# Kernel optimization log

Hardware: AMD Instinct MI355X
Metric: run time of the kernel (lower is better)

Reference implementation:

```python
import jax, jax.numpy as jnp
import numpy as np

B, S, HID = 1, 2048, 2048
H, KVH, HD = 32, 8, 64
THETA = 10000.0


def _rotate_half(x):
    x1, x2 = jnp.split(x, 2, axis=-1)
    return jnp.concatenate([-x2, x1], axis=-1)


def _rope_cos_sin(seq_len, head_dim, theta, dtype):
    inv_freq = 1.0 / (theta ** (jnp.arange(0, head_dim, 2, dtype=jnp.float32) / head_dim))
    pos = jnp.arange(seq_len, dtype=jnp.float32)
    freqs = pos[:, None] * inv_freq[None, :]          # [S, HD/2]
    emb = jnp.concatenate([freqs, freqs], axis=-1)     # [S, HD]
    return jnp.cos(emb).astype(dtype), jnp.sin(emb).astype(dtype)


def setup_inputs() -> dict:
    key = jax.random.key(0)
    k0, k1, k2, k3, k4 = jax.random.split(key, 5)
    w = lambda k, shape: jax.random.normal(k, shape, dtype=jnp.float32) * 0.02
    return {
        "hidden_states": jax.random.normal(k0, (B, S, HID), dtype=jnp.float32),
        "Wq": w(k1, (H * HD, HID)),
        "Wk": w(k2, (KVH * HD, HID)),
        "Wv": w(k3, (KVH * HD, HID)),
        "Wo": w(k4, (HID, H * HD)),
    }


def reference(hidden_states, Wq, Wk, Wv, Wo):
    b, s, _ = hidden_states.shape
    dtype = hidden_states.dtype

    # QKV projections (nn.Linear, bias=False -> x @ W.T)
    q = (hidden_states @ Wq.T).reshape(b, s, H, HD).transpose(0, 2, 1, 3)    # [b,H,s,d]
    k = (hidden_states @ Wk.T).reshape(b, s, KVH, HD).transpose(0, 2, 1, 3)  # [b,KVH,s,d]
    v = (hidden_states @ Wv.T).reshape(b, s, KVH, HD).transpose(0, 2, 1, 3)

    # RoPE (prefill: position_ids = arange(s))
    cos, sin = _rope_cos_sin(s, HD, THETA, dtype)  # [s, HD]
    apply_rope = lambda x: x * cos + _rotate_half(x) * sin
    q = apply_rope(q)
    k = apply_rope(k)

    # GQA: repeat KV heads to match query heads
    groups = H // KVH
    k = jnp.repeat(k, groups, axis=1)  # [b,H,s,d]
    v = jnp.repeat(v, groups, axis=1)

    scale = 1.0 / jnp.sqrt(jnp.asarray(HD, dtype=dtype))
    logits = jnp.einsum('bhqd,bhkd->bhqk', q, k) * scale  # [b,H,s,s]

    # prefill causal mask (phys_past_len = 0)
    causal = jnp.tril(jnp.ones((s, s), dtype=bool))
    logits = jnp.where(causal, logits, jnp.finfo(dtype).min)

    attn = jax.nn.softmax(logits, axis=-1)
    out = jnp.einsum('bhqk,bhkd->bhqd', attn, v)            # [b,H,s,d]
    out = out.transpose(0, 2, 1, 3).reshape(b, s, H * HD)   # [b,s,hidden]
    return out @ Wo.T
```

## Files before the change

kernel.cpp:

```cpp
#include <hip/hip_runtime.h>
#include <hip/hip_bf16.h>
#include <cstdint>
#include <cstddef>

#define SEQ   2048
#define HID   2048
#define NH    32
#define NKVH  8
#define HD    64
#define KVDIM (NKVH * HD)

typedef __bf16 bf16_t;
typedef __bf16 bf16x8 __attribute__((ext_vector_type(8)));
typedef float  f32x4  __attribute__((ext_vector_type(4)));

#define ROPE_L 0.4152410118609203f

#if __has_builtin(__builtin_amdgcn_exp2f)
#define QSCALE 0.18033688011112043f
#define EXPFN(x) __builtin_amdgcn_exp2f(x)
#else
#define QSCALE 0.125f
#define EXPFN(x) __expf(x)
#endif

__device__ __forceinline__ bf16x8 load8(const float* p) {
    const float4 lo = *(const float4*)p;
    const float4 hi = *(const float4*)(p + 4);
    bf16x8 r;
    r[0] = (bf16_t)lo.x; r[1] = (bf16_t)lo.y; r[2] = (bf16_t)lo.z; r[3] = (bf16_t)lo.w;
    r[4] = (bf16_t)hi.x; r[5] = (bf16_t)hi.y; r[6] = (bf16_t)hi.z; r[7] = (bf16_t)hi.w;
    return r;
}

__device__ __forceinline__ void load_lds16(const bf16_t* g, bf16_t* l) {
    __builtin_amdgcn_global_load_lds((const __attribute__((address_space(1))) void*)g,
                                     (__attribute__((address_space(3))) void*)l,
                                     16, 0, 0);
}

#define NX  (SEQ * HID)
#define NWQ (NH * HD * HID)
#define NWK (KVDIM * HID)
#define NWV (KVDIM * HID)
#define NWO (HID * NH * HD)
#define NTOT (NX + NWQ + NWK + NWV + NWO)

__global__ __launch_bounds__(256) void cvt_all(const float* __restrict__ X,
                                               const float* __restrict__ Wq,
                                               const float* __restrict__ Wk,
                                               const float* __restrict__ Wv,
                                               const float* __restrict__ Wo,
                                               bf16_t* __restrict__ Xb,
                                               bf16_t* __restrict__ Wqb,
                                               bf16_t* __restrict__ Wkb,
                                               bf16_t* __restrict__ Wvb,
                                               bf16_t* __restrict__ Wob)
{
    size_t i = ((size_t)blockIdx.x * 256 + threadIdx.x) * 8;
    if (i >= NTOT) return;
    const size_t E0 = NX, E1 = E0 + NWQ, E2 = E1 + NWK, E3 = E2 + NWV;
    const float* s; bf16_t* d; size_t off;
    if (i < E0)      { s = X;  d = Xb;  off = i; }
    else if (i < E1) { s = Wq; d = Wqb; off = i - E0; }
    else if (i < E2) { s = Wk; d = Wkb; off = i - E1; }
    else if (i < E3) { s = Wv; d = Wvb; off = i - E2; }
    else             { s = Wo; d = Wob; off = i - E3; }
    *(bf16x8*)(d + off) = load8(s + off);
}

__global__ __launch_bounds__(256) void qkv_gemm(const bf16_t* __restrict__ Xb,
                                                const bf16_t* __restrict__ Wqb,
                                                const bf16_t* __restrict__ Wkb,
                                                const bf16_t* __restrict__ Wvb,
                                                bf16_t* __restrict__ Qb,
                                                bf16_t* __restrict__ Kb,
                                                bf16_t* __restrict__ Vt)
{
    __shared__ alignas(16) bf16_t sa[128 * 32];
    __shared__ alignas(16) bf16_t sb[64 * 32];
    const int t = threadIdx.x;
    const int lane = t & 63;
    const int w  = t >> 6;
    const int n16 = lane & 15;
    const int q4  = lane >> 4;
    f32x4 acc[2][4] = {};

    const int m0 = blockIdx.x * 128;
    const int n0 = blockIdx.y * 64;

    const bf16_t* B;
    int mode, nc;
    if (n0 < NH * HD)              { B = Wqb + (size_t)n0 * HID;                     mode = 0; nc = n0; }
    else if (n0 < NH * HD + KVDIM) { B = Wkb + (size_t)(n0 - NH * HD) * HID;         mode = 1; nc = n0 - NH * HD; }
    else                           { B = Wvb + (size_t)(n0 - NH * HD - KVDIM) * HID; mode = 2; nc = n0 - NH * HD - KVDIM; }

    const int lrow = lane >> 2;
    const int lcol = (lane & 3) * 8;
    const bf16_t* ag = Xb + (size_t)(m0 + w * 32 + lrow) * HID + lcol;
    const bf16_t* bg = B  + (size_t)(w * 16 + lrow) * HID + lcol;
    bf16_t* la0 = &sa[(w * 32) * 32];
    bf16_t* la1 = &sa[(w * 32 + 16) * 32];
    bf16_t* lb0 = &sb[(w * 16) * 32];

    for (int k0 = 0; k0 < HID; k0 += 32) {
        load_lds16(ag + k0, la0);
        load_lds16(ag + k0 + (size_t)16 * HID, la1);
        load_lds16(bg + k0, lb0);
        __syncthreads();
        bf16x8 bfrag[4];
#pragma unroll
        for (int j = 0; j < 4; ++j)
            bfrag[j] = *(const bf16x8*)&sb[(j * 16 + n16) * 32 + q4 * 8];
#pragma unroll
        for (int i = 0; i < 2; ++i) {
            bf16x8 af = *(const bf16x8*)&sa[(w * 32 + i * 16 + n16) * 32 + q4 * 8];
#pragma unroll
            for (int j = 0; j < 4; ++j)
                acc[i][j] = __builtin_amdgcn_mfma_f32_16x16x32_bf16(af, bfrag[j], acc[i][j], 0, 0, 0);
        }
        __syncthreads();
    }

    if (mode < 2) {
#pragma unroll
        for (int jt = 0; jt < 2; ++jt) {
            float dd = (float)(jt * 16 + n16);
            float inv = exp2f(-dd * ROPE_L);
#pragma unroll
            for (int i = 0; i < 2; ++i) {
#pragma unroll
                for (int r = 0; r < 4; ++r) {
                    int pos = m0 + w * 32 + i * 16 + q4 * 4 + r;
                    float ang = (float)pos * inv;
                    float sn, cs;
                    sincosf(ang, &sn, &cs);
                    float x1 = acc[i][jt][r], x2 = acc[i][jt + 2][r];
                    acc[i][jt][r]     = x1 * cs - x2 * sn;
                    acc[i][jt + 2][r] = x2 * cs + x1 * sn;
                }
            }
        }
        const float osc = (mode == 0) ? QSCALE : 1.0f;
        bf16_t* dst = (mode == 0) ? Qb : Kb;
        const int ld = (mode == 0) ? NH * HD : KVDIM;
#pragma unroll
        for (int i = 0; i < 2; ++i)
#pragma unroll
            for (int j = 0; j < 4; ++j) {
                int row = m0 + w * 32 + i * 16 + q4 * 4;
                int col = nc + j * 16 + n16;
#pragma unroll
                for (int r = 0; r < 4; ++r)
                    dst[(size_t)(row + r) * ld + col] = (bf16_t)(acc[i][j][r] * osc);
            }
    } else {
#pragma unroll
        for (int i = 0; i < 2; ++i)
#pragma unroll
            for (int j = 0; j < 4; ++j) {
                int row = m0 + w * 32 + i * 16 + q4 * 4;
                int col = nc + j * 16 + n16;
#pragma unroll
                for (int r = 0; r < 4; ++r)
                    Vt[(size_t)col * SEQ + row + r] = (bf16_t)acc[i][j][r];
            }
    }
}

__global__ __launch_bounds__(256) void o_gemm(const bf16_t* __restrict__ A,
                                              const bf16_t* __restrict__ Bw,
                                              float* __restrict__ C)
{
    __shared__ alignas(16) bf16_t sa[128 * 32];
    __shared__ alignas(16) bf16_t sb[64 * 32];
    const int t = threadIdx.x;
    const int lane = t & 63;
    const int w  = t >> 6;
    const int n16 = lane & 15;
    const int q4  = lane >> 4;
    f32x4 acc[2][4] = {};

    const int m0 = blockIdx.x * 128;
    const int n0 = blockIdx.y * 64;

    const int lrow = lane >> 2;
    const int lcol = (lane & 3) * 8;
    const bf16_t* ag = A  + (size_t)(m0 + w * 32 + lrow) * HID + lcol;
    const bf16_t* bg = Bw + (size_t)(n0 + w * 16 + lrow) * HID + lcol;
    bf16_t* la0 = &sa[(w * 32) * 32];
    bf16_t* la1 = &sa[(w * 32 + 16) * 32];
    bf16_t* lb0 = &sb[(w * 16) * 32];

    for (int k0 = 0; k0 < HID; k0 += 32) {
        load_lds16(ag + k0, la0);
        load_lds16(ag + k0 + (size_t)16 * HID, la1);
        load_lds16(bg + k0, lb0);
        __syncthreads();
        bf16x8 bfrag[4];
#pragma unroll
        for (int j = 0; j < 4; ++j)
            bfrag[j] = *(const bf16x8*)&sb[(j * 16 + n16) * 32 + q4 * 8];
#pragma unroll
        for (int i = 0; i < 2; ++i) {
            bf16x8 af = *(const bf16x8*)&sa[(w * 32 + i * 16 + n16) * 32 + q4 * 8];
#pragma unroll
            for (int j = 0; j < 4; ++j)
                acc[i][j] = __builtin_amdgcn_mfma_f32_16x16x32_bf16(af, bfrag[j], acc[i][j], 0, 0, 0);
        }
        __syncthreads();
    }

#pragma unroll
    for (int i = 0; i < 2; ++i)
#pragma unroll
        for (int j = 0; j < 4; ++j) {
            int row = m0 + w * 32 + i * 16 + q4 * 4;
            int col = n0 + j * 16 + n16;
#pragma unroll
            for (int r = 0; r < 4; ++r)
                C[(size_t)(row + r) * HID + col] = acc[i][j][r];
        }
}

__global__ __launch_bounds__(256) void attn_mfma(const bf16_t* __restrict__ Qm,
                                                 const bf16_t* __restrict__ Km,
                                                 const bf16_t* __restrict__ Vt,
                                                 bf16_t* __restrict__ Om)
{
    const int h   = blockIdx.x & (NH - 1);
    const int qt  = (SEQ / 64 - 1) - (blockIdx.x >> 5);
    const int q0  = qt * 64;
    const int kvh = h >> 2;
    const int t   = threadIdx.x;
    const int w   = t >> 6;
    const int lane = t & 63;
    const int n16 = lane & 15;
    const int q4  = lane >> 4;

    __shared__ alignas(16) bf16_t kA[128 * 32];
    __shared__ alignas(16) bf16_t kB[128 * 32];
    __shared__ alignas(16) bf16_t vc0[64 * 32], vc1[64 * 32];
    __shared__ alignas(16) bf16_t vc2[64 * 32], vc3[64 * 32];
    __shared__ alignas(16) bf16_t psA[4][16 * 32];
    __shared__ alignas(16) bf16_t psB[4][16 * 32];

    const int qrow = q0 + w * 16 + n16;
    const bf16_t* qbase = Qm + (size_t)qrow * HID + h * HD;
    const bf16x8 qf0 = *(const bf16x8*)(qbase + q4 * 8);
    const bf16x8 qf1 = *(const bf16x8*)(qbase + 32 + q4 * 8);

    f32x4 acc[4] = {};
    f32x4 acc_l = {};
    const bf16_t one = (bf16_t)1.0f;
    const bf16x8 ones8 = {one, one, one, one, one, one, one, one};

    const int srow = lane >> 2;
    const int scol = (lane & 3) * 8;
    const bf16_t* kg = Km + (size_t)kvh * HD + scol;
    const bf16_t* vg = Vt + (size_t)(kvh * HD) * SEQ;

    const int rowg0 = q0 + w * 16 + q4 * 4;
    const int nhalf = qt + 1;

    for (int kb = 0; kb * 2 < nhalf; ++kb) {
        const int k0 = kb * 128;
        {
            const int r0 = w * 16 + srow;
            const bf16_t* kp0 = kg + (size_t)(k0 + r0) * KVDIM;
            const bf16_t* kp1 = kg + (size_t)(k0 + 64 + r0) * KVDIM;
            load_lds16(kp0,      &kA[(w * 16) * 32]);
            load_lds16(kp0 + 32, &kB[(w * 16) * 32]);
            load_lds16(kp1,      &kA[(64 + w * 16) * 32]);
            load_lds16(kp1 + 32, &kB[(64 + w * 16) * 32]);
            const bf16_t* vp = vg + (size_t)r0 * SEQ + k0 + scol;
            load_lds16(vp,      &vc0[(w * 16) * 32]);
            load_lds16(vp + 32, &vc1[(w * 16) * 32]);
            load_lds16(vp + 64, &vc2[(w * 16) * 32]);
            load_lds16(vp + 96, &vc3[(w * 16) * 32]);
        }
        __syncthreads();

#pragma unroll
        for (int hh = 0; hh < 2; ++hh) {
            const int gh = 2 * kb + hh;
            if (gh >= nhalf) break;
            const bf16_t* kAh = &kA[hh * 64 * 32];
            const bf16_t* kBh = &kB[hh * 64 * 32];
            const bf16_t* vAh = hh ? vc2 : vc0;
            const bf16_t* vBh = hh ? vc3 : vc1;

            f32x4 st[4];
#pragma unroll
            for (int jt = 0; jt < 4; ++jt) {
                bf16x8 kf0 = *(const bf16x8*)&kAh[(jt * 16 + n16) * 32 + q4 * 8];
                bf16x8 kf1 = *(const bf16x8*)&kBh[(jt * 16 + n16) * 32 + q4 * 8];
                f32x4 s = {};
                s = __builtin_amdgcn_mfma_f32_16x16x32_bf16(qf0, kf0, s, 0, 0, 0);
                s = __builtin_amdgcn_mfma_f32_16x16x32_bf16(qf1, kf1, s, 0, 0, 0);
                st[jt] = s;
            }

            if (gh == qt) {
#pragma unroll
                for (int jt = 0; jt < 4; ++jt) {
                    int colg = gh * 64 + jt * 16 + n16;
#pragma unroll
                    for (int r = 0; r < 4; ++r)
                        if (colg > rowg0 + r) st[jt][r] = -1e30f;
                }
            }

#pragma unroll
            for (int jt = 0; jt < 4; ++jt)
#pragma unroll
                for (int r = 0; r < 4; ++r)
                    st[jt][r] = EXPFN(st[jt][r]);

#pragma unroll
            for (int jt = 0; jt < 4; ++jt) {
                bf16_t* ph = (jt < 2) ? psA[w] : psB[w];
                int c16 = (jt & 1) * 16;
#pragma unroll
                for (int r = 0; r < 4; ++r)
                    ph[(q4 * 4 + r) * 32 + c16 + n16] = (bf16_t)st[jt][r];
            }
            bf16x8 pf0 = *(const bf16x8*)&psA[w][n16 * 32 + q4 * 8];
            bf16x8 pf1 = *(const bf16x8*)&psB[w][n16 * 32 + q4 * 8];

            acc_l = __builtin_amdgcn_mfma_f32_16x16x32_bf16(pf0, ones8, acc_l, 0, 0, 0);
            acc_l = __builtin_amdgcn_mfma_f32_16x16x32_bf16(pf1, ones8, acc_l, 0, 0, 0);

#pragma unroll
            for (int jd = 0; jd < 4; ++jd) {
                bf16x8 vf0 = *(const bf16x8*)&vAh[(jd * 16 + n16) * 32 + q4 * 8];
                bf16x8 vf1 = *(const bf16x8*)&vBh[(jd * 16 + n16) * 32 + q4 * 8];
                acc[jd] = __builtin_amdgcn_mfma_f32_16x16x32_bf16(pf0, vf0, acc[jd], 0, 0, 0);
                acc[jd] = __builtin_amdgcn_mfma_f32_16x16x32_bf16(pf1, vf1, acc[jd], 0, 0, 0);
            }
        }
        __syncthreads();
    }

    float linv[4];
#pragma unroll
    for (int r = 0; r < 4; ++r) linv[r] = 1.0f / acc_l[r];
#pragma unroll
    for (int jd = 0; jd < 4; ++jd)
#pragma unroll
        for (int r = 0; r < 4; ++r) {
            int rowg = rowg0 + r;
            Om[(size_t)rowg * HID + h * HD + jd * 16 + n16] = (bf16_t)(acc[jd][r] * linv[r]);
        }
}

extern "C" void kernel_launch(void* const* d_in, const int* in_sizes, int n_in,
                              void* d_out, int out_size, void* d_ws, size_t ws_size,
                              hipStream_t stream)
{
    const float* X  = (const float*)d_in[0];
    const float* Wq = (const float*)d_in[1];
    const float* Wk = (const float*)d_in[2];
    const float* Wv = (const float*)d_in[3];
    const float* Wo = (const float*)d_in[4];
    float* out = (float*)d_out;

    bf16_t* Xb  = (bf16_t*)d_ws;
    bf16_t* Wqb = Xb  + (size_t)NX;
    bf16_t* Wkb = Wqb + (size_t)NWQ;
    bf16_t* Wvb = Wkb + (size_t)NWK;
    bf16_t* Wob = Wvb + (size_t)NWV;
    bf16_t* Qb  = Wob + (size_t)NWO;
    bf16_t* Kb  = Qb  + (size_t)SEQ * (NH * HD);
    bf16_t* Vt  = Kb  + (size_t)SEQ * KVDIM;
    bf16_t* Ob  = Vt  + (size_t)SEQ * KVDIM;

    dim3 blk(256);

    cvt_all<<<dim3((NTOT / 8 + 255) / 256), blk, 0, stream>>>(X, Wq, Wk, Wv, Wo, Xb, Wqb, Wkb, Wvb, Wob);

    qkv_gemm<<<dim3(SEQ / 128, (NH * HD + 2 * KVDIM) / 64), blk, 0, stream>>>(Xb, Wqb, Wkb, Wvb, Qb, Kb, Vt);

    attn_mfma<<<dim3((SEQ / 64) * NH), blk, 0, stream>>>(Qb, Kb, Vt, Ob);

    o_gemm<<<dim3(SEQ / 128, HID / 64), blk, 0, stream>>>(Ob, Wob, out);
}
```

Measured before the change: 214.7 us.

## Double K-step in GEMMs and use 128-row query tiles in attention

Both GEMMs now stage 64 columns of K per barrier pair, in two LDS sub-buffers, which halves the number of __syncthreads per tile. Attention now handles 128 query rows per block with 32 rows per wave, so each K/V tile loaded into LDS serves twice as many queries. It also interleaves long and short causal tiles in the block order to balance load, and swizzles the P staging buffer to cut LDS bank conflicts. The costs are more LDS and registers per block and fewer blocks overall, which launch_bounds(256,3) tries to keep at an acceptable occupancy.

```diff
diff --git a/kernel.cpp b/kernel.cpp
--- a/kernel.cpp
+++ b/kernel.cpp
@@ -77,8 +77,8 @@
                                                 bf16_t* __restrict__ Kb,
                                                 bf16_t* __restrict__ Vt)
 {
-    __shared__ alignas(16) bf16_t sa[128 * 32];
-    __shared__ alignas(16) bf16_t sb[64 * 32];
+    __shared__ alignas(16) bf16_t sa0[128 * 32], sa1[128 * 32];
+    __shared__ alignas(16) bf16_t sb0[64 * 32],  sb1[64 * 32];
     const int t = threadIdx.x;
     const int lane = t & 63;
     const int w  = t >> 6;
@@ -97,27 +97,38 @@
 
     const int lrow = lane >> 2;
     const int lcol = (lane & 3) * 8;
-    const bf16_t* ag = Xb + (size_t)(m0 + w * 32 + lrow) * HID + lcol;
+    const bf16_t* ag = Xb + (size_t)(m0 + w * 16 + lrow) * HID + lcol;
     const bf16_t* bg = B  + (size_t)(w * 16 + lrow) * HID + lcol;
-    bf16_t* la0 = &sa[(w * 32) * 32];
-    bf16_t* la1 = &sa[(w * 32 + 16) * 32];
-    bf16_t* lb0 = &sb[(w * 16) * 32];
-
-    for (int k0 = 0; k0 < HID; k0 += 32) {
-        load_lds16(ag + k0, la0);
-        load_lds16(ag + k0 + (size_t)16 * HID, la1);
-        load_lds16(bg + k0, lb0);
-        __syncthreads();
-        bf16x8 bfrag[4];
-#pragma unroll
-        for (int j = 0; j < 4; ++j)
-            bfrag[j] = *(const bf16x8*)&sb[(j * 16 + n16) * 32 + q4 * 8];
-#pragma unroll
-        for (int i = 0; i < 2; ++i) {
-            bf16x8 af = *(const bf16x8*)&sa[(w * 32 + i * 16 + n16) * 32 + q4 * 8];
+    bf16_t* la0  = &sa0[(w * 16) * 32];
+    bf16_t* la1  = &sa1[(w * 16) * 32];
+    bf16_t* la0b = &sa0[(64 + w * 16) * 32];
+    bf16_t* la1b = &sa1[(64 + w * 16) * 32];
+    bf16_t* lb0  = &sb0[(w * 16) * 32];
+    bf16_t* lb1  = &sb1[(w * 16) * 32];
+
+    for (int k0 = 0; k0 < HID; k0 += 64) {
+        load_lds16(ag + k0,                        la0);
+        load_lds16(ag + k0 + 32,                   la1);
+        load_lds16(ag + (size_t)64 * HID + k0,      la0b);
+        load_lds16(ag + (size_t)64 * HID + k0 + 32, la1b);
+        load_lds16(bg + k0,      lb0);
+        load_lds16(bg + k0 + 32, lb1);
+        __syncthreads();
+#pragma unroll
+        for (int kk = 0; kk < 2; ++kk) {
+            const bf16_t* sa = kk ? sa1 : sa0;
+            const bf16_t* sb = kk ? sb1 : sb0;
+            bf16x8 bfrag[4];
 #pragma unroll
             for (int j = 0; j < 4; ++j)
-                acc[i][j] = __builtin_amdgcn_mfma_f32_16x16x32_bf16(af, bfrag[j], acc[i][j], 0, 0, 0);
+                bfrag[j] = *(const bf16x8*)&sb[(j * 16 + n16) * 32 + q4 * 8];
+#pragma unroll
+            for (int i = 0; i < 2; ++i) {
+                bf16x8 af = *(const bf16x8*)&sa[(w * 32 + i * 16 + n16) * 32 + q4 * 8];
+#pragma unroll
+                for (int j = 0; j < 4; ++j)
+                    acc[i][j] = __builtin_amdgcn_mfma_f32_16x16x32_bf16(af, bfrag[j], acc[i][j], 0, 0, 0);
+            }
         }
         __syncthreads();
     }
@@ -172,8 +183,8 @@
                                               const bf16_t* __restrict__ Bw,
                                               float* __restrict__ C)
 {
-    __shared__ alignas(16) bf16_t sa[128 * 32];
-    __shared__ alignas(16) bf16_t sb[64 * 32];
+    __shared__ alignas(16) bf16_t sa0[128 * 32], sa1[128 * 32];
+    __shared__ alignas(16) bf16_t sb0[64 * 32],  sb1[64 * 32];
     const int t = threadIdx.x;
     const int lane = t & 63;
     const int w  = t >> 6;
@@ -186,27 +197,38 @@
 
     const int lrow = lane >> 2;
     const int lcol = (lane & 3) * 8;
-    const bf16_t* ag = A  + (size_t)(m0 + w * 32 + lrow) * HID + lcol;
+    const bf16_t* ag = A  + (size_t)(m0 + w * 16 + lrow) * HID + lcol;
     const bf16_t* bg = Bw + (size_t)(n0 + w * 16 + lrow) * HID + lcol;
-    bf16_t* la0 = &sa[(w * 32) * 32];
-    bf16_t* la1 = &sa[(w * 32 + 16) * 32];
-    bf16_t* lb0 = &sb[(w * 16) * 32];
-
-    for (int k0 = 0; k0 < HID; k0 += 32) {
-        load_lds16(ag + k0, la0);
-        load_lds16(ag + k0 + (size_t)16 * HID, la1);
-        load_lds16(bg + k0, lb0);
-        __syncthreads();
-        bf16x8 bfrag[4];
-#pragma unroll
-        for (int j = 0; j < 4; ++j)
-            bfrag[j] = *(const bf16x8*)&sb[(j * 16 + n16) * 32 + q4 * 8];
-#pragma unroll
-        for (int i = 0; i < 2; ++i) {
-            bf16x8 af = *(const bf16x8*)&sa[(w * 32 + i * 16 + n16) * 32 + q4 * 8];
+    bf16_t* la0  = &sa0[(w * 16) * 32];
+    bf16_t* la1  = &sa1[(w * 16) * 32];
+    bf16_t* la0b = &sa0[(64 + w * 16) * 32];
+    bf16_t* la1b = &sa1[(64 + w * 16) * 32];
+    bf16_t* lb0  = &sb0[(w * 16) * 32];
+    bf16_t* lb1  = &sb1[(w * 16) * 32];
+
+    for (int k0 = 0; k0 < HID; k0 += 64) {
+        load_lds16(ag + k0,                        la0);
+        load_lds16(ag + k0 + 32,                   la1);
+        load_lds16(ag + (size_t)64 * HID + k0,      la0b);
+        load_lds16(ag + (size_t)64 * HID + k0 + 32, la1b);
+        load_lds16(bg + k0,      lb0);
+        load_lds16(bg + k0 + 32, lb1);
+        __syncthreads();
+#pragma unroll
+        for (int kk = 0; kk < 2; ++kk) {
+            const bf16_t* sa = kk ? sa1 : sa0;
+            const bf16_t* sb = kk ? sb1 : sb0;
+            bf16x8 bfrag[4];
 #pragma unroll
             for (int j = 0; j < 4; ++j)
-                acc[i][j] = __builtin_amdgcn_mfma_f32_16x16x32_bf16(af, bfrag[j], acc[i][j], 0, 0, 0);
+                bfrag[j] = *(const bf16x8*)&sb[(j * 16 + n16) * 32 + q4 * 8];
+#pragma unroll
+            for (int i = 0; i < 2; ++i) {
+                bf16x8 af = *(const bf16x8*)&sa[(w * 32 + i * 16 + n16) * 32 + q4 * 8];
+#pragma unroll
+                for (int j = 0; j < 4; ++j)
+                    acc[i][j] = __builtin_amdgcn_mfma_f32_16x16x32_bf16(af, bfrag[j], acc[i][j], 0, 0, 0);
+            }
         }
         __syncthreads();
     }
@@ -223,35 +245,40 @@
         }
 }
 
-__global__ __launch_bounds__(256) void attn_mfma(const bf16_t* __restrict__ Qm,
-                                                 const bf16_t* __restrict__ Km,
-                                                 const bf16_t* __restrict__ Vt,
-                                                 bf16_t* __restrict__ Om)
+__global__ __launch_bounds__(256, 3) void attn_mfma(const bf16_t* __restrict__ Qm,
+                                                    const bf16_t* __restrict__ Km,
+                                                    const bf16_t* __restrict__ Vt,
+                                                    bf16_t* __restrict__ Om)
 {
-    const int h   = blockIdx.x & (NH - 1);
-    const int qt  = (SEQ / 64 - 1) - (blockIdx.x >> 5);
-    const int q0  = qt * 64;
+    const int bid = blockIdx.x;
+    const int h   = bid & (NH - 1);
+    const int qt  = (bid < (SEQ / 128) * NH / 2)
+                      ? (SEQ / 128 - 1 - (bid >> 5))
+                      : ((bid - (SEQ / 128) * NH / 2) >> 5);
+    const int q0  = qt * 128;
     const int kvh = h >> 2;
-    const int t   = threadIdx.x;
-    const int w   = t >> 6;
+    const int t    = threadIdx.x;
+    const int w    = t >> 6;
     const int lane = t & 63;
-    const int n16 = lane & 15;
-    const int q4  = lane >> 4;
+    const int n16  = lane & 15;
+    const int q4   = lane >> 4;
 
     __shared__ alignas(16) bf16_t kA[128 * 32];
     __shared__ alignas(16) bf16_t kB[128 * 32];
     __shared__ alignas(16) bf16_t vc0[64 * 32], vc1[64 * 32];
     __shared__ alignas(16) bf16_t vc2[64 * 32], vc3[64 * 32];
-    __shared__ alignas(16) bf16_t psA[4][16 * 32];
-    __shared__ alignas(16) bf16_t psB[4][16 * 32];
-
-    const int qrow = q0 + w * 16 + n16;
-    const bf16_t* qbase = Qm + (size_t)qrow * HID + h * HD;
-    const bf16x8 qf0 = *(const bf16x8*)(qbase + q4 * 8);
-    const bf16x8 qf1 = *(const bf16x8*)(qbase + 32 + q4 * 8);
-
-    f32x4 acc[4] = {};
-    f32x4 acc_l = {};
+    __shared__ alignas(16) bf16_t ps[4][2][32 * 40];
+
+    bf16x8 qf[2][2];
+#pragma unroll
+    for (int i = 0; i < 2; ++i) {
+        const bf16_t* qp = Qm + (size_t)(q0 + w * 32 + i * 16 + n16) * HID + h * HD;
+        qf[i][0] = *(const bf16x8*)(qp + q4 * 8);
+        qf[i][1] = *(const bf16x8*)(qp + 32 + q4 * 8);
+    }
+
+    f32x4 acc[2][4] = {};
+    f32x4 acc_l[2] = {};
     const bf16_t one = (bf16_t)1.0f;
     const bf16x8 ones8 = {one, one, one, one, one, one, one, one};
 
@@ -260,10 +287,11 @@
     const bf16_t* kg = Km + (size_t)kvh * HD + scol;
     const bf16_t* vg = Vt + (size_t)(kvh * HD) * SEQ;
 
-    const int rowg0 = q0 + w * 16 + q4 * 4;
-    const int nhalf = qt + 1;
-
-    for (int kb = 0; kb * 2 < nhalf; ++kb) {
+    const int my_last = 2 * qt + (w >> 1);
+    const int wkey   = (q4 & 2) << 3;
+    const int rdkey  = ((n16 >> 2) & 2) << 3;
+
+    for (int kb = 0; kb <= qt; ++kb) {
         const int k0 = kb * 128;
         {
             const int r0 = w * 16 + srow;
@@ -281,77 +309,103 @@
         }
         __syncthreads();
 
-#pragma unroll
         for (int hh = 0; hh < 2; ++hh) {
             const int gh = 2 * kb + hh;
-            if (gh >= nhalf) break;
+            if (gh > my_last) break;
             const bf16_t* kAh = &kA[hh * 64 * 32];
             const bf16_t* kBh = &kB[hh * 64 * 32];
             const bf16_t* vAh = hh ? vc2 : vc0;
             const bf16_t* vBh = hh ? vc3 : vc1;
 
-            f32x4 st[4];
+            f32x4 st[2][4];
 #pragma unroll
             for (int jt = 0; jt < 4; ++jt) {
                 bf16x8 kf0 = *(const bf16x8*)&kAh[(jt * 16 + n16) * 32 + q4 * 8];
                 bf16x8 kf1 = *(const bf16x8*)&kBh[(jt * 16 + n16) * 32 + q4 * 8];
-                f32x4 s = {};
-                s = __builtin_amdgcn_mfma_f32_16x16x32_bf16(qf0, kf0, s, 0, 0, 0);
-                s = __builtin_amdgcn_mfma_f32_16x16x32_bf16(qf1, kf1, s, 0, 0, 0);
-                st[jt] = s;
-            }
-
-            if (gh == qt) {
+#pragma unroll
+                for (int i = 0; i < 2; ++i) {
+                    f32x4 s = {};
+                    s = __builtin_amdgcn_mfma_f32_16x16x32_bf16(qf[i][0], kf0, s, 0, 0, 0);
+                    s = __builtin_amdgcn_mfma_f32_16x16x32_bf16(qf[i][1], kf1, s, 0, 0, 0);
+                    st[i][jt] = s;
+                }
+            }
+
+            if (gh == my_last) {
+#pragma unroll
+                for (int i = 0; i < 2; ++i) {
+                    int rowb = q0 + w * 32 + i * 16 + q4 * 4;
+#pragma unroll
+                    for (int jt = 0; jt < 4; ++jt) {
+                        int colg = gh * 64 + jt * 16 + n16;
+#pragma unroll
+                        for (int r = 0; r < 4; ++r)
+                            if (colg > rowb + r) st[i][jt][r] = -1e30f;
+                    }
+                }
+            }
+
+#pragma unroll
+            for (int i = 0; i < 2; ++i)
+#pragma unroll
+                for (int jt = 0; jt < 4; ++jt)
+#pragma unroll
+                    for (int r = 0; r < 4; ++r)
+                        st[i][jt][r] = EXPFN(st[i][jt][r]);
+
+#pragma unroll
+            for (int i = 0; i < 2; ++i)
 #pragma unroll
                 for (int jt = 0; jt < 4; ++jt) {
-                    int colg = gh * 64 + jt * 16 + n16;
+                    bf16_t* ph = ps[w][jt >> 1];
+                    int rowb = i * 16 + q4 * 4;
+                    int csw  = ((jt & 1) * 16 + n16) ^ wkey;
 #pragma unroll
                     for (int r = 0; r < 4; ++r)
-                        if (colg > rowg0 + r) st[jt][r] = -1e30f;
+                        ph[(rowb + r) * 40 + csw] = (bf16_t)st[i][jt][r];
                 }
-            }
-
-#pragma unroll
-            for (int jt = 0; jt < 4; ++jt)
-#pragma unroll
-                for (int r = 0; r < 4; ++r)
-                    st[jt][r] = EXPFN(st[jt][r]);
-
-#pragma unroll
-            for (int jt = 0; jt < 4; ++jt) {
-                bf16_t* ph = (jt < 2) ? psA[w] : psB[w];
-                int c16 = (jt & 1) * 16;
-#pragma unroll
-                for (int r = 0; r < 4; ++r)
-                    ph[(q4 * 4 + r) * 32 + c16 + n16] = (bf16_t)st[jt][r];
-            }
-            bf16x8 pf0 = *(const bf16x8*)&psA[w][n16 * 32 + q4 * 8];
-            bf16x8 pf1 = *(const bf16x8*)&psB[w][n16 * 32 + q4 * 8];
-
-            acc_l = __builtin_amdgcn_mfma_f32_16x16x32_bf16(pf0, ones8, acc_l, 0, 0, 0);
-            acc_l = __builtin_amdgcn_mfma_f32_16x16x32_bf16(pf1, ones8, acc_l, 0, 0, 0);
+
+            bf16x8 pf[2][2];
+#pragma unroll
+            for (int i = 0; i < 2; ++i) {
+                int ra = (i * 16 + n16) * 40 + ((q4 * 8) ^ rdkey);
+                pf[i][0] = *(const bf16x8*)&ps[w][0][ra];
+                pf[i][1] = *(const bf16x8*)&ps[w][1][ra];
+            }
+
+#pragma unroll
+            for (int i = 0; i < 2; ++i) {
+                acc_l[i] = __builtin_amdgcn_mfma_f32_16x16x32_bf16(pf[i][0], ones8, acc_l[i], 0, 0, 0);
+                acc_l[i] = __builtin_amdgcn_mfma_f32_16x16x32_bf16(pf[i][1], ones8, acc_l[i], 0, 0, 0);
+            }
 
 #pragma unroll
             for (int jd = 0; jd < 4; ++jd) {
                 bf16x8 vf0 = *(const bf16x8*)&vAh[(jd * 16 + n16) * 32 + q4 * 8];
                 bf16x8 vf1 = *(const bf16x8*)&vBh[(jd * 16 + n16) * 32 + q4 * 8];
-                acc[jd] = __builtin_amdgcn_mfma_f32_16x16x32_bf16(pf0, vf0, acc[jd], 0, 0, 0);
-                acc[jd] = __builtin_amdgcn_mfma_f32_16x16x32_bf16(pf1, vf1, acc[jd], 0, 0, 0);
-            }
-        }
-        __syncthreads();
-    }
-
-    float linv[4];
-#pragma unroll
-    for (int r = 0; r < 4; ++r) linv[r] = 1.0f / acc_l[r];
-#pragma unroll
-    for (int jd = 0; jd < 4; ++jd)
-#pragma unroll
-        for (int r = 0; r < 4; ++r) {
-            int rowg = rowg0 + r;
-            Om[(size_t)rowg * HID + h * HD + jd * 16 + n16] = (bf16_t)(acc[jd][r] * linv[r]);
-        }
+#pragma unroll
+                for (int i = 0; i < 2; ++i) {
+                    acc[i][jd] = __builtin_amdgcn_mfma_f32_16x16x32_bf16(pf[i][0], vf0, acc[i][jd], 0, 0, 0);
+                    acc[i][jd] = __builtin_amdgcn_mfma_f32_16x16x32_bf16(pf[i][1], vf1, acc[i][jd], 0, 0, 0);
+                }
+            }
+        }
+        __syncthreads();
+    }
+
+#pragma unroll
+    for (int i = 0; i < 2; ++i) {
+        float linv[4];
+#pragma unroll
+        for (int r = 0; r < 4; ++r) linv[r] = 1.0f / acc_l[i][r];
+#pragma unroll
+        for (int jd = 0; jd < 4; ++jd)
+#pragma unroll
+            for (int r = 0; r < 4; ++r) {
+                int rowg = q0 + w * 32 + i * 16 + q4 * 4 + r;
+                Om[(size_t)rowg * HID + h * HD + jd * 16 + n16] = (bf16_t)(acc[i][jd][r] * linv[r]);
+            }
+    }
 }
 
 extern "C" void kernel_launch(void* const* d_in, const int* in_sizes, int n_in,
@@ -381,7 +435,7 @@
 
     qkv_gemm<<<dim3(SEQ / 128, (NH * HD + 2 * KVDIM) / 64), blk, 0, stream>>>(Xb, Wqb, Wkb, Wvb, Qb, Kb, Vt);
 
-    attn_mfma<<<dim3((SEQ / 64) * NH), blk, 0, stream>>>(Qb, Kb, Vt, Ob);
+    attn_mfma<<<dim3((SEQ / 128) * NH), blk, 0, stream>>>(Qb, Kb, Vt, Ob);
 
     o_gemm<<<dim3(SEQ / 128, HID / 64), blk, 0, stream>>>(Ob, Wob, out);
 }
```

Measured after the change: 210.9 us. Within noise of the previous version (-1.8%).
